# Kernel tuning notes

Measured on AMD Instinct MI355X. Metric: run time of the kernel, lower is better.

## Reference

```python
import jax, jax.numpy as jnp
import numpy as np

B, S, D, H = 2, 2048, 2048, 16
HD = D // H  # head_dim = 128
THETA = 10000.0


def _rope(x, sin, cos):
    # x: [b,h,s,hd]; rotate-half convention: cat(-x2, x1)
    d = x.shape[-1] // 2
    x1, x2 = x[..., :d], x[..., d:]
    x_rot = jnp.concatenate([-x2, x1], axis=-1)
    return x * cos + x_rot * sin


def setup_inputs() -> dict:
    key = jax.random.key(0)
    k0, k1, k2 = jax.random.split(key, 3)
    x = jax.random.normal(k0, (B, S, D), jnp.float32)
    Wqkv = jax.random.normal(k1, (D, 3 * D), jnp.float32) * 0.02
    Wproj = jax.random.normal(k2, (D, D), jnp.float32) * 0.02
    # causal mask [1,1,S,S]
    mask = jnp.tril(jnp.ones((S, S), jnp.int32))[None, None]
    # rotary tables [1,1,S,HD]
    inv_freq = 1.0 / (THETA ** (np.arange(0, HD, 2, dtype=np.float64) / HD))
    freqs = np.outer(np.arange(S, dtype=np.float64), inv_freq)
    emb = np.concatenate([freqs, freqs], axis=-1)
    sin = jnp.asarray(np.sin(emb), jnp.float32)[None, None]
    cos = jnp.asarray(np.cos(emb), jnp.float32)[None, None]
    return {"x": x, "mask": mask, "sin": sin, "cos": cos, "Wqkv": Wqkv, "Wproj": Wproj}


def reference(x, mask, sin, cos, Wqkv, Wproj):
    b, s, d = x.shape
    qkv = (x @ Wqkv).reshape(b, s, 3, H, HD).transpose(2, 0, 3, 1, 4)  # [3,b,h,s,hd]
    q, k, v = qkv[0], qkv[1], qkv[2]
    q = _rope(q, sin[:, :, :s, :], cos[:, :, :s, :])
    k = _rope(k, sin[:, :, :s, :], cos[:, :, :s, :])
    att = jnp.einsum('bhqd,bhkd->bhqk', q, k) / jnp.sqrt(jnp.float32(HD))
    att = jnp.where(mask == 0, -jnp.inf, att)
    probs = jax.nn.softmax(att, axis=-1)
    out = jnp.einsum('bhqk,bhkd->bhqd', probs, v)
    out = out.transpose(0, 2, 1, 3).reshape(b, s, d)
    return out @ Wproj
```

## Files before the change

kernel.cpp:

```cpp
#include <hip/hip_runtime.h>
#include <hip/hip_bf16.h>
#include <stdint.h>

#define B_ 2
#define S_ 2048
#define D_ 2048
#define H_ 16
#define HD_ 128
#define N3_ 6144

typedef __attribute__((ext_vector_type(8))) short short8;
typedef __attribute__((ext_vector_type(4))) float f32x4;
typedef __hip_bfloat16 bf16;

__global__ void cast_bf16_kernel(const float* __restrict__ in, bf16* __restrict__ out, int n4) {
  int i = blockIdx.x * blockDim.x + threadIdx.x;
  if (i >= n4) return;
  float4 v = ((const float4*)in)[i];
  bf16 a = __float2bfloat16(v.x), b = __float2bfloat16(v.y);
  bf16 c = __float2bfloat16(v.z), d = __float2bfloat16(v.w);
  ushort4 o;
  o.x = *(unsigned short*)&a; o.y = *(unsigned short*)&b;
  o.z = *(unsigned short*)&c; o.w = *(unsigned short*)&d;
  ((ushort4*)out)[i] = o;
}

__global__ void transpose_cast_kernel(const float* __restrict__ in, bf16* __restrict__ out,
                                      int R, int C) {
  __shared__ float tile[32][33];
  int c0 = blockIdx.x * 32, r0 = blockIdx.y * 32;
  int tx = threadIdx.x, ty = threadIdx.y;
#pragma unroll
  for (int i = 0; i < 4; i++)
    tile[ty + i * 8][tx] = in[(size_t)(r0 + ty + i * 8) * C + c0 + tx];
  __syncthreads();
#pragma unroll
  for (int i = 0; i < 4; i++) {
    int oc = ty + i * 8;
    out[(size_t)(c0 + oc) * R + r0 + tx] = __float2bfloat16(tile[tx][oc]);
  }
}

__device__ __forceinline__ void store_c(float* p, float v) { *p = v; }
__device__ __forceinline__ void store_c(bf16* p, float v) { *p = __float2bfloat16(v); }

template <typename CT>
__global__ __launch_bounds__(256, 2) void gemm_bt_kernel(
    const bf16* __restrict__ A, const bf16* __restrict__ Bt, CT* __restrict__ C,
    int M, int N, int K) {
  __shared__ bf16 a_lds[128 * 64];
  __shared__ bf16 b_lds[128 * 64];
  int t = threadIdx.x;
  int lane = t & 63, w = t >> 6;
  int lane15 = lane & 15, quad = lane >> 4;
  int wm = w >> 1, wn = w & 1;
  int m0 = blockIdx.y * 128, n0 = blockIdx.x * 128;

  f32x4 acc[4][4];
#pragma unroll
  for (int i = 0; i < 4; i++)
#pragma unroll
    for (int j = 0; j < 4; j++) acc[i][j] = (f32x4){0.f, 0.f, 0.f, 0.f};

  const bf16* ga = A + (size_t)m0 * K;
  const bf16* gb = Bt + (size_t)n0 * K;

  int sr[4], sgc[4];
#pragma unroll
  for (int i = 0; i < 4; i++) {
    int ch = t + i * 256;
    sr[i] = ch >> 3;
    sgc[i] = (ch & 7) ^ (sr[i] & 7);
  }
  int sx = lane15 & 7;

  for (int kt = 0; kt < K; kt += 64) {
    __syncthreads();
#pragma unroll
    for (int i = 0; i < 4; i++) {
      int ch = t + i * 256;
      __builtin_amdgcn_global_load_lds(
          (const __attribute__((address_space(1))) void*)(ga + (size_t)sr[i] * K + kt + sgc[i] * 8),
          (__attribute__((address_space(3))) void*)(a_lds + ch * 8), 16, 0, 0);
      __builtin_amdgcn_global_load_lds(
          (const __attribute__((address_space(1))) void*)(gb + (size_t)sr[i] * K + kt + sgc[i] * 8),
          (__attribute__((address_space(3))) void*)(b_lds + ch * 8), 16, 0, 0);
    }
    __syncthreads();

#pragma unroll
    for (int ks = 0; ks < 2; ks++) {
      int slot = (ks * 4 + quad) ^ sx;
      short8 af[4], bfr[4];
#pragma unroll
      for (int mt = 0; mt < 4; mt++)
        af[mt] = *(const short8*)(a_lds + (wm * 64 + mt * 16 + lane15) * 64 + slot * 8);
#pragma unroll
      for (int nt = 0; nt < 4; nt++)
        bfr[nt] = *(const short8*)(b_lds + (wn * 64 + nt * 16 + lane15) * 64 + slot * 8);
#pragma unroll
      for (int mt = 0; mt < 4; mt++)
#pragma unroll
        for (int nt = 0; nt < 4; nt++)
          acc[mt][nt] = __builtin_amdgcn_mfma_f32_16x16x32_bf16(af[mt], bfr[nt], acc[mt][nt], 0, 0, 0);
    }
  }

#pragma unroll
  for (int mt = 0; mt < 4; mt++)
#pragma unroll
    for (int nt = 0; nt < 4; nt++)
#pragma unroll
      for (int r = 0; r < 4; r++) {
        int row = m0 + wm * 64 + mt * 16 + quad * 4 + r;
        int col = n0 + wn * 64 + nt * 16 + lane15;
        store_c(&C[(size_t)row * N + col], acc[mt][nt][r]);
      }
}

__global__ void rope_qk_kernel(const bf16* __restrict__ qkv, const float* __restrict__ sinp,
                               const float* __restrict__ cosp, bf16* __restrict__ Q,
                               bf16* __restrict__ K) {
  int bs = blockIdx.x;
  int b = bs >> 11, s = bs & 2047;
  const bf16* row = qkv + (size_t)bs * N3_;
  for (int p = threadIdx.x; p < 2048; p += 256) {
    int g = p >> 10;
    int pp = p & 1023;
    int h = pp >> 6, i = pp & 63;
    float x1 = __bfloat162float(row[g * D_ + h * HD_ + i]);
    float x2 = __bfloat162float(row[g * D_ + h * HD_ + i + 64]);
    float sn = sinp[s * HD_ + i];
    float cs = cosp[s * HD_ + i];
    float o1 = x1 * cs - x2 * sn;
    float o2 = x2 * cs + x1 * sn;
    bf16* dst = (g == 0) ? Q : K;
    size_t base = (((size_t)b * H_ + h) * S_ + s) * HD_;
    dst[base + i] = __float2bfloat16(o1);
    dst[base + i + 64] = __float2bfloat16(o2);
  }
}

__global__ void transpose_v_kernel(const bf16* __restrict__ qkv, bf16* __restrict__ Vt) {
  __shared__ __align__(16) bf16 tile[64][HD_ + 8];
  int bh = blockIdx.y;
  int b = bh >> 4, h = bh & 15;
  int s0 = blockIdx.x * 64;
  int t = threadIdx.x;
#pragma unroll
  for (int i = 0; i < 4; i++) {
    int ch = t + i * 256;
    int r = ch >> 4, cc = (ch & 15) * 8;
    *(uint4*)&tile[r][cc] =
        *(const uint4*)(qkv + (size_t)(b * S_ + s0 + r) * N3_ + 2 * D_ + h * HD_ + cc);
  }
  __syncthreads();
#pragma unroll
  for (int i = 0; i < 4; i++) {
    int ch = t + i * 256;
    int hd = ch >> 3, sl = (ch & 7) * 8;
    union { bf16 v[8]; uint4 u; } tmp;
#pragma unroll
    for (int j = 0; j < 8; j++) tmp.v[j] = tile[sl + j][hd];
    *(uint4*)(Vt + (((size_t)b * H_ + h) * HD_ + hd) * S_ + s0 + sl) = tmp.u;
  }
}

__global__ __launch_bounds__(256, 1) void attn_kernel(
    const bf16* __restrict__ Q, const bf16* __restrict__ K, const bf16* __restrict__ Vt,
    bf16* __restrict__ Out) {
  __shared__ __align__(16) bf16 k_lds[2][64 * HD_];
  __shared__ __align__(16) bf16 v_lds[2][HD_ * 64];
  __shared__ __align__(16) bf16 p_lds[4][32][64 + 8];
  const float SCALE_LOG2 = 0.08838834764831845f * 1.4426950408889634f;

  int bh = blockIdx.x;
  int b = bh >> 4, h = bh & 15;
  int t = threadIdx.x, w = t >> 6, lane = t & 63;
  int lane15 = lane & 15, quad = lane >> 4;

  const bf16* Qb = Q + ((size_t)b * H_ + h) * S_ * HD_;
  const bf16* Kb = K + ((size_t)b * H_ + h) * S_ * HD_;
  const bf16* Vb = Vt + ((size_t)b * H_ + h) * HD_ * S_;

  int kr[4], kgc[4], vr[4], vgc[4];
#pragma unroll
  for (int i = 0; i < 4; i++) {
    int ch = t + i * 256;
    kr[i] = ch >> 4; kgc[i] = (ch & 15) ^ (kr[i] & 15);
    vr[i] = ch >> 3; vgc[i] = (ch & 7) ^ (vr[i] & 7);
  }

  auto issue_kv = [&](int kv0, int bufi) {
#pragma unroll
    for (int i = 0; i < 4; i++) {
      int ch = t + i * 256;
      __builtin_amdgcn_global_load_lds(
          (const __attribute__((address_space(1))) void*)(Kb + (size_t)(kv0 + kr[i]) * HD_ + kgc[i] * 8),
          (__attribute__((address_space(3))) void*)(&k_lds[bufi][ch * 8]), 16, 0, 0);
      __builtin_amdgcn_global_load_lds(
          (const __attribute__((address_space(1))) void*)(Vb + (size_t)vr[i] * S_ + kv0 + vgc[i] * 8),
          (__attribute__((address_space(3))) void*)(&v_lds[bufi][ch * 8]), 16, 0, 0);
    }
  };

#pragma unroll 1
  for (int ph = 0; ph < 2; ph++) {
    int qi = ph ? (15 - (int)blockIdx.y) : (int)blockIdx.y;
    int q0 = qi * 128;
    int ntiles = 2 * qi + 2;

    short8 qf[2][4];
#pragma unroll
    for (int mt = 0; mt < 2; mt++) {
      int qrow = q0 + w * 32 + mt * 16 + lane15;
#pragma unroll
      for (int k0 = 0; k0 < 4; k0++)
        qf[mt][k0] = *(const short8*)(Qb + (size_t)qrow * HD_ + k0 * 32 + quad * 8);
    }

    f32x4 o_acc[2][8];
#pragma unroll
    for (int mt = 0; mt < 2; mt++)
#pragma unroll
      for (int i = 0; i < 8; i++) o_acc[mt][i] = (f32x4){0.f, 0.f, 0.f, 0.f};
    float m_run[2][4], l_run[2][4];
#pragma unroll
    for (int mt = 0; mt < 2; mt++)
#pragma unroll
      for (int r = 0; r < 4; r++) { m_run[mt][r] = -1e30f; l_run[mt][r] = 0.f; }
    int row_base[2];
    row_base[0] = q0 + w * 32 + quad * 4;
    row_base[1] = q0 + w * 32 + 16 + quad * 4;

    issue_kv(0, 0);

#pragma unroll 1
    for (int tk = 0; tk < ntiles; tk++) {
      int cur = tk & 1;
      int kv0 = tk * 64;
      if (tk + 1 < ntiles) {
        issue_kv(kv0 + 64, cur ^ 1);
        __builtin_amdgcn_s_waitcnt(0xF78);
      } else {
        __builtin_amdgcn_s_waitcnt(0xF70);
      }
      __builtin_amdgcn_s_barrier();

      const bf16* kb = k_lds[cur];
      const bf16* vb = v_lds[cur];
      bool masked = (tk >= 2 * qi);

#pragma unroll
      for (int mt = 0; mt < 2; mt++) {
        f32x4 s_acc[4];
#pragma unroll
        for (int nt = 0; nt < 4; nt++) {
          f32x4 acc = (f32x4){0.f, 0.f, 0.f, 0.f};
#pragma unroll
          for (int k0 = 0; k0 < 4; k0++) {
            int r2 = nt * 16 + lane15;
            int cch = (k0 * 4 + quad) ^ (r2 & 15);
            short8 kf = *(const short8*)(kb + r2 * HD_ + cch * 8);
            acc = __builtin_amdgcn_mfma_f32_16x16x32_bf16(qf[mt][k0], kf, acc, 0, 0, 0);
          }
          s_acc[nt] = acc;
        }

        float p[4][4];
        float rowmax[4] = {-1e30f, -1e30f, -1e30f, -1e30f};
#pragma unroll
        for (int nt = 0; nt < 4; nt++) {
          int col = kv0 + nt * 16 + lane15;
#pragma unroll
          for (int r = 0; r < 4; r++) {
            float v = s_acc[nt][r] * SCALE_LOG2;
            if (masked && col > row_base[mt] + r) v = -1e30f;
            p[nt][r] = v;
            rowmax[r] = fmaxf(rowmax[r], v);
          }
        }
        float alpha[4];
#pragma unroll
        for (int r = 0; r < 4; r++) {
          float v = rowmax[r];
          v = fmaxf(v, __shfl_xor(v, 1));
          v = fmaxf(v, __shfl_xor(v, 2));
          v = fmaxf(v, __shfl_xor(v, 4));
          v = fmaxf(v, __shfl_xor(v, 8));
          float mnew = fmaxf(m_run[mt][r], v);
          alpha[r] = __builtin_amdgcn_exp2f(m_run[mt][r] - mnew);
          m_run[mt][r] = mnew;
        }
#pragma unroll
        for (int r = 0; r < 4; r++) {
          float lsum = 0.f;
#pragma unroll
          for (int nt = 0; nt < 4; nt++) {
            float e = __builtin_amdgcn_exp2f(p[nt][r] - m_run[mt][r]);
            p[nt][r] = e;
            lsum += e;
          }
          l_run[mt][r] = l_run[mt][r] * alpha[r] + lsum;
        }
#pragma unroll
        for (int on = 0; on < 8; on++) {
          f32x4 o = o_acc[mt][on];
          o[0] *= alpha[0]; o[1] *= alpha[1]; o[2] *= alpha[2]; o[3] *= alpha[3];
          o_acc[mt][on] = o;
        }
#pragma unroll
        for (int nt = 0; nt < 4; nt++)
#pragma unroll
          for (int r = 0; r < 4; r++)
            p_lds[w][mt * 16 + quad * 4 + r][nt * 16 + lane15] = __float2bfloat16(p[nt][r]);
      }

#pragma unroll
      for (int mt = 0; mt < 2; mt++)
#pragma unroll
        for (int k0 = 0; k0 < 2; k0++) {
          short8 pf = *(const short8*)&p_lds[w][mt * 16 + lane15][k0 * 32 + quad * 8];
#pragma unroll
          for (int on = 0; on < 8; on++) {
            int rv = on * 16 + lane15;
            int cch = (k0 * 4 + quad) ^ (rv & 7);
            short8 vf = *(const short8*)(v_lds[cur] + rv * 64 + cch * 8);
            o_acc[mt][on] = __builtin_amdgcn_mfma_f32_16x16x32_bf16(pf, vf, o_acc[mt][on], 0, 0, 0);
          }
        }

      __builtin_amdgcn_s_barrier();
    }

#pragma unroll
    for (int mt = 0; mt < 2; mt++) {
#pragma unroll
      for (int r = 0; r < 4; r++) {
        float v = l_run[mt][r];
        v += __shfl_xor(v, 1);
        v += __shfl_xor(v, 2);
        v += __shfl_xor(v, 4);
        v += __shfl_xor(v, 8);
        l_run[mt][r] = 1.f / v;
      }
#pragma unroll
      for (int on = 0; on < 8; on++)
#pragma unroll
        for (int r = 0; r < 4; r++) {
          int s = row_base[mt] + r;
          Out[((size_t)(b * S_ + s)) * D_ + h * HD_ + on * 16 + lane15] =
              __float2bfloat16(o_acc[mt][on][r] * l_run[mt][r]);
        }
    }
  }
}

extern "C" void kernel_launch(void* const* d_in, const int* in_sizes, int n_in,
                              void* d_out, int out_size, void* d_ws, size_t ws_size,
                              hipStream_t stream) {
  const float* x = (const float*)d_in[0];
  const float* sinp = (const float*)d_in[2];
  const float* cosp = (const float*)d_in[3];
  const float* Wqkv = (const float*)d_in[4];
  const float* Wproj = (const float*)d_in[5];
  float* out = (float*)d_out;

  char* ws = (char*)d_ws;
  bf16* x_bf = (bf16*)ws;    ws += (size_t)B_ * S_ * D_ * 2;
  bf16* wqkv_t = (bf16*)ws;  ws += (size_t)N3_ * D_ * 2;
  bf16* wproj_t = (bf16*)ws; ws += (size_t)D_ * D_ * 2;
  bf16* qkv = (bf16*)ws;     ws += (size_t)B_ * S_ * N3_ * 2;
  bf16* Qp = (bf16*)ws;      ws += (size_t)B_ * S_ * D_ * 2;
  bf16* Kp = (bf16*)ws;      ws += (size_t)B_ * S_ * D_ * 2;
  bf16* Vt = (bf16*)ws;      ws += (size_t)B_ * S_ * D_ * 2;
  bf16* attn = (bf16*)ws;    ws += (size_t)B_ * S_ * D_ * 2;

  int nx4 = B_ * S_ * D_ / 4;
  cast_bf16_kernel<<<nx4 / 256, 256, 0, stream>>>(x, x_bf, nx4);
  transpose_cast_kernel<<<dim3(N3_ / 32, D_ / 32), dim3(32, 8), 0, stream>>>(Wqkv, wqkv_t, D_, N3_);
  transpose_cast_kernel<<<dim3(D_ / 32, D_ / 32), dim3(32, 8), 0, stream>>>(Wproj, wproj_t, D_, D_);

  gemm_bt_kernel<bf16><<<dim3(N3_ / 128, (B_ * S_) / 128), 256, 0, stream>>>(
      x_bf, wqkv_t, qkv, B_ * S_, N3_, D_);

  rope_qk_kernel<<<B_ * S_, 256, 0, stream>>>(qkv, sinp, cosp, Qp, Kp);
  transpose_v_kernel<<<dim3(S_ / 64, B_ * H_), 256, 0, stream>>>(qkv, Vt);

  attn_kernel<<<dim3(B_ * H_, S_ / 128 / 2), 256, 0, stream>>>(Qp, Kp, Vt, attn);

  gemm_bt_kernel<float><<<dim3(D_ / 128, (B_ * S_) / 128), 256, 0, stream>>>(
      attn, wproj_t, out, B_ * S_, D_, D_);
}
```

Before: 434.1 us.

## Use 8 waves per attention block with 16 query rows each

```diff
diff --git a/kernel.cpp b/kernel.cpp
--- a/kernel.cpp
+++ b/kernel.cpp
@@ -166,12 +166,12 @@
   }
 }
 
-__global__ __launch_bounds__(256, 1) void attn_kernel(
+__global__ __launch_bounds__(512, 1) void attn_kernel(
     const bf16* __restrict__ Q, const bf16* __restrict__ K, const bf16* __restrict__ Vt,
     bf16* __restrict__ Out) {
   __shared__ __align__(16) bf16 k_lds[2][64 * HD_];
   __shared__ __align__(16) bf16 v_lds[2][HD_ * 64];
-  __shared__ __align__(16) bf16 p_lds[4][32][64 + 8];
+  __shared__ __align__(16) bf16 p_lds[8][16][64 + 8];
   const float SCALE_LOG2 = 0.08838834764831845f * 1.4426950408889634f;
 
   int bh = blockIdx.x;
@@ -183,18 +183,18 @@
   const bf16* Kb = K + ((size_t)b * H_ + h) * S_ * HD_;
   const bf16* Vb = Vt + ((size_t)b * H_ + h) * HD_ * S_;
 
-  int kr[4], kgc[4], vr[4], vgc[4];
-#pragma unroll
-  for (int i = 0; i < 4; i++) {
-    int ch = t + i * 256;
+  int kr[2], kgc[2], vr[2], vgc[2];
+#pragma unroll
+  for (int i = 0; i < 2; i++) {
+    int ch = t + i * 512;
     kr[i] = ch >> 4; kgc[i] = (ch & 15) ^ (kr[i] & 15);
     vr[i] = ch >> 3; vgc[i] = (ch & 7) ^ (vr[i] & 7);
   }
 
   auto issue_kv = [&](int kv0, int bufi) {
 #pragma unroll
-    for (int i = 0; i < 4; i++) {
-      int ch = t + i * 256;
+    for (int i = 0; i < 2; i++) {
+      int ch = t + i * 512;
       __builtin_amdgcn_global_load_lds(
           (const __attribute__((address_space(1))) void*)(Kb + (size_t)(kv0 + kr[i]) * HD_ + kgc[i] * 8),
           (__attribute__((address_space(3))) void*)(&k_lds[bufi][ch * 8]), 16, 0, 0);
@@ -210,28 +210,21 @@
     int q0 = qi * 128;
     int ntiles = 2 * qi + 2;
 
-    short8 qf[2][4];
-#pragma unroll
-    for (int mt = 0; mt < 2; mt++) {
-      int qrow = q0 + w * 32 + mt * 16 + lane15;
+    short8 qf[4];
+    {
+      int qrow = q0 + w * 16 + lane15;
 #pragma unroll
       for (int k0 = 0; k0 < 4; k0++)
-        qf[mt][k0] = *(const short8*)(Qb + (size_t)qrow * HD_ + k0 * 32 + quad * 8);
-    }
-
-    f32x4 o_acc[2][8];
-#pragma unroll
-    for (int mt = 0; mt < 2; mt++)
-#pragma unroll
-      for (int i = 0; i < 8; i++) o_acc[mt][i] = (f32x4){0.f, 0.f, 0.f, 0.f};
-    float m_run[2][4], l_run[2][4];
-#pragma unroll
-    for (int mt = 0; mt < 2; mt++)
-#pragma unroll
-      for (int r = 0; r < 4; r++) { m_run[mt][r] = -1e30f; l_run[mt][r] = 0.f; }
-    int row_base[2];
-    row_base[0] = q0 + w * 32 + quad * 4;
-    row_base[1] = q0 + w * 32 + 16 + quad * 4;
+        qf[k0] = *(const short8*)(Qb + (size_t)qrow * HD_ + k0 * 32 + quad * 8);
+    }
+
+    f32x4 o_acc[8];
+#pragma unroll
+    for (int i = 0; i < 8; i++) o_acc[i] = (f32x4){0.f, 0.f, 0.f, 0.f};
+    float m_run[4], l_run[4];
+#pragma unroll
+    for (int r = 0; r < 4; r++) { m_run[r] = -1e30f; l_run[r] = 0.f; }
+    int row_base = q0 + w * 16 + quad * 4;
 
     issue_kv(0, 0);
 
@@ -241,118 +234,109 @@
       int kv0 = tk * 64;
       if (tk + 1 < ntiles) {
         issue_kv(kv0 + 64, cur ^ 1);
-        __builtin_amdgcn_s_waitcnt(0xF78);
+        __builtin_amdgcn_s_waitcnt(0xF74);
       } else {
         __builtin_amdgcn_s_waitcnt(0xF70);
       }
       __builtin_amdgcn_s_barrier();
 
       const bf16* kb = k_lds[cur];
-      const bf16* vb = v_lds[cur];
       bool masked = (tk >= 2 * qi);
 
-#pragma unroll
-      for (int mt = 0; mt < 2; mt++) {
-        f32x4 s_acc[4];
+      f32x4 s_acc[4];
+#pragma unroll
+      for (int nt = 0; nt < 4; nt++) {
+        f32x4 acc = (f32x4){0.f, 0.f, 0.f, 0.f};
+#pragma unroll
+        for (int k0 = 0; k0 < 4; k0++) {
+          int r2 = nt * 16 + lane15;
+          int cch = (k0 * 4 + quad) ^ (r2 & 15);
+          short8 kf = *(const short8*)(kb + r2 * HD_ + cch * 8);
+          acc = __builtin_amdgcn_mfma_f32_16x16x32_bf16(qf[k0], kf, acc, 0, 0, 0);
+        }
+        s_acc[nt] = acc;
+      }
+
+      float p[4][4];
+      float rowmax[4] = {-1e30f, -1e30f, -1e30f, -1e30f};
+#pragma unroll
+      for (int nt = 0; nt < 4; nt++) {
+        int col = kv0 + nt * 16 + lane15;
+#pragma unroll
+        for (int r = 0; r < 4; r++) {
+          float v = s_acc[nt][r] * SCALE_LOG2;
+          if (masked && col > row_base + r) v = -1e30f;
+          p[nt][r] = v;
+          rowmax[r] = fmaxf(rowmax[r], v);
+        }
+      }
+      float alpha[4];
+#pragma unroll
+      for (int r = 0; r < 4; r++) {
+        float v = rowmax[r];
+        v = fmaxf(v, __shfl_xor(v, 1));
+        v = fmaxf(v, __shfl_xor(v, 2));
+        v = fmaxf(v, __shfl_xor(v, 4));
+        v = fmaxf(v, __shfl_xor(v, 8));
+        float mnew = fmaxf(m_run[r], v);
+        alpha[r] = __builtin_amdgcn_exp2f(m_run[r] - mnew);
+        m_run[r] = mnew;
+      }
+#pragma unroll
+      for (int r = 0; r < 4; r++) {
+        float lsum = 0.f;
 #pragma unroll
         for (int nt = 0; nt < 4; nt++) {
-          f32x4 acc = (f32x4){0.f, 0.f, 0.f, 0.f};
-#pragma unroll
-          for (int k0 = 0; k0 < 4; k0++) {
-            int r2 = nt * 16 + lane15;
-            int cch = (k0 * 4 + quad) ^ (r2 & 15);
-            short8 kf = *(const short8*)(kb + r2 * HD_ + cch * 8);
-            acc = __builtin_amdgcn_mfma_f32_16x16x32_bf16(qf[mt][k0], kf, acc, 0, 0, 0);
-          }
-          s_acc[nt] = acc;
+          float e = __builtin_amdgcn_exp2f(p[nt][r] - m_run[r]);
+          p[nt][r] = e;
+          lsum += e;
         }
-
-        float p[4][4];
-        float rowmax[4] = {-1e30f, -1e30f, -1e30f, -1e30f};
-#pragma unroll
-        for (int nt = 0; nt < 4; nt++) {
-          int col = kv0 + nt * 16 + lane15;
-#pragma unroll
-          for (int r = 0; r < 4; r++) {
-            float v = s_acc[nt][r] * SCALE_LOG2;
-            if (masked && col > row_base[mt] + r) v = -1e30f;
-            p[nt][r] = v;
-            rowmax[r] = fmaxf(rowmax[r], v);
-          }
+        l_run[r] = l_run[r] * alpha[r] + lsum;
+      }
+#pragma unroll
+      for (int on = 0; on < 8; on++) {
+        f32x4 o = o_acc[on];
+        o[0] *= alpha[0]; o[1] *= alpha[1]; o[2] *= alpha[2]; o[3] *= alpha[3];
+        o_acc[on] = o;
+      }
+#pragma unroll
+      for (int nt = 0; nt < 4; nt++)
+#pragma unroll
+        for (int r = 0; r < 4; r++)
+          p_lds[w][quad * 4 + r][nt * 16 + lane15] = __float2bfloat16(p[nt][r]);
+
+#pragma unroll
+      for (int k0 = 0; k0 < 2; k0++) {
+        short8 pf = *(const short8*)&p_lds[w][lane15][k0 * 32 + quad * 8];
+#pragma unroll
+        for (int on = 0; on < 8; on++) {
+          int rv = on * 16 + lane15;
+          int cch = (k0 * 4 + quad) ^ (rv & 7);
+          short8 vf = *(const short8*)(v_lds[cur] + rv * 64 + cch * 8);
+          o_acc[on] = __builtin_amdgcn_mfma_f32_16x16x32_bf16(pf, vf, o_acc[on], 0, 0, 0);
         }
-        float alpha[4];
-#pragma unroll
-        for (int r = 0; r < 4; r++) {
-          float v = rowmax[r];
-          v = fmaxf(v, __shfl_xor(v, 1));
-          v = fmaxf(v, __shfl_xor(v, 2));
-          v = fmaxf(v, __shfl_xor(v, 4));
-          v = fmaxf(v, __shfl_xor(v, 8));
-          float mnew = fmaxf(m_run[mt][r], v);
-          alpha[r] = __builtin_amdgcn_exp2f(m_run[mt][r] - mnew);
-          m_run[mt][r] = mnew;
-        }
-#pragma unroll
-        for (int r = 0; r < 4; r++) {
-          float lsum = 0.f;
-#pragma unroll
-          for (int nt = 0; nt < 4; nt++) {
-            float e = __builtin_amdgcn_exp2f(p[nt][r] - m_run[mt][r]);
-            p[nt][r] = e;
-            lsum += e;
-          }
-          l_run[mt][r] = l_run[mt][r] * alpha[r] + lsum;
-        }
-#pragma unroll
-        for (int on = 0; on < 8; on++) {
-          f32x4 o = o_acc[mt][on];
-          o[0] *= alpha[0]; o[1] *= alpha[1]; o[2] *= alpha[2]; o[3] *= alpha[3];
-          o_acc[mt][on] = o;
-        }
-#pragma unroll
-        for (int nt = 0; nt < 4; nt++)
-#pragma unroll
-          for (int r = 0; r < 4; r++)
-            p_lds[w][mt * 16 + quad * 4 + r][nt * 16 + lane15] = __float2bfloat16(p[nt][r]);
-      }
-
-#pragma unroll
-      for (int mt = 0; mt < 2; mt++)
-#pragma unroll
-        for (int k0 = 0; k0 < 2; k0++) {
-          short8 pf = *(const short8*)&p_lds[w][mt * 16 + lane15][k0 * 32 + quad * 8];
-#pragma unroll
-          for (int on = 0; on < 8; on++) {
-            int rv = on * 16 + lane15;
-            int cch = (k0 * 4 + quad) ^ (rv & 7);
-            short8 vf = *(const short8*)(v_lds[cur] + rv * 64 + cch * 8);
-            o_acc[mt][on] = __builtin_amdgcn_mfma_f32_16x16x32_bf16(pf, vf, o_acc[mt][on], 0, 0, 0);
-          }
-        }
+      }
 
       __builtin_amdgcn_s_barrier();
     }
 
 #pragma unroll
-    for (int mt = 0; mt < 2; mt++) {
+    for (int r = 0; r < 4; r++) {
+      float v = l_run[r];
+      v += __shfl_xor(v, 1);
+      v += __shfl_xor(v, 2);
+      v += __shfl_xor(v, 4);
+      v += __shfl_xor(v, 8);
+      l_run[r] = 1.f / v;
+    }
+#pragma unroll
+    for (int on = 0; on < 8; on++)
 #pragma unroll
       for (int r = 0; r < 4; r++) {
-        float v = l_run[mt][r];
-        v += __shfl_xor(v, 1);
-        v += __shfl_xor(v, 2);
-        v += __shfl_xor(v, 4);
-        v += __shfl_xor(v, 8);
-        l_run[mt][r] = 1.f / v;
-      }
-#pragma unroll
-      for (int on = 0; on < 8; on++)
-#pragma unroll
-        for (int r = 0; r < 4; r++) {
-          int s = row_base[mt] + r;
-          Out[((size_t)(b * S_ + s)) * D_ + h * HD_ + on * 16 + lane15] =
-              __float2bfloat16(o_acc[mt][on][r] * l_run[mt][r]);
-        }
-    }
+        int s = row_base + r;
+        Out[((size_t)(b * S_ + s)) * D_ + h * HD_ + on * 16 + lane15] =
+            __float2bfloat16(o_acc[on][r] * l_run[r]);
+      }
   }
 }
 
@@ -387,7 +371,7 @@
   rope_qk_kernel<<<B_ * S_, 256, 0, stream>>>(qkv, sinp, cosp, Qp, Kp);
   transpose_v_kernel<<<dim3(S_ / 64, B_ * H_), 256, 0, stream>>>(qkv, Vt);
 
-  attn_kernel<<<dim3(B_ * H_, S_ / 128 / 2), 256, 0, stream>>>(Qp, Kp, Vt, attn);
+  attn_kernel<<<dim3(B_ * H_, S_ / 128 / 2), 512, 0, stream>>>(Qp, Kp, Vt, attn);
 
   gemm_bt_kernel<float><<<dim3(D_ / 128, (B_ * S_) / 128), 256, 0, stream>>>(
       attn, wproj_t, out, B_ * S_, D_, D_);
```

Result: faster. 388.2 us (-10.6%).
